# Kernel optimization log

Hardware: AMD Instinct MI355X
Metric: run time of the kernel (lower is better)

The kernel has to match this reference:

```python
import jax, jax.numpy as jnp
import numpy as np

N = 100_000   # number of local objects (rows of h_local)
E = 800_000   # number of edges (objects of class 'branch')
D = 64        # local hidden dim / out_size
DG = 16       # global hidden dim
FL = 4        # local features per edge
FG = 4        # global features
H = 128       # MLP hidden size


def setup_inputs() -> dict:
    key = jax.random.key(0)
    ks = jax.random.split(key, 20)
    inp = {}
    inp["addr_from"] = jax.random.randint(ks[0], (E,), 0, N)
    inp["addr_to"] = jax.random.randint(ks[1], (E,), 0, N)
    inp["h_local"] = jax.random.normal(ks[2], (N, D), dtype=jnp.float32)
    inp["h_global"] = jax.random.normal(ks[3], (1, DG), dtype=jnp.float32)
    inp["x_local"] = jax.random.normal(ks[4], (E, FL), dtype=jnp.float32)
    inp["x_global"] = jax.random.normal(ks[5], (1, FG), dtype=jnp.float32)
    inp["t"] = jax.random.uniform(ks[6], (1, 1), dtype=jnp.float32)
    din = 2 * D + FL + DG + FG + 1  # concat of [h_from, h_to, x_v, h_g, x_g, t]
    dims = [din, H, H, D]
    i = 7
    for pfx in ("f", "t"):  # one MLP per address field: 'from' and 'to'
        for l in range(3):
            w = (jax.random.normal(ks[i], (dims[l], dims[l + 1])) / np.sqrt(dims[l])).astype(jnp.float32)
            i += 1
            inp[f"{pfx}_W{l}"] = w
            inp[f"{pfx}_b{l}"] = jnp.zeros((dims[l + 1],), jnp.float32)
    return inp


def _mlp(x, W0, b0, W1, b1, W2, b2):
    # MLP: Dense->tanh for each hidden layer, final Dense without activation
    x = jnp.tanh(x @ W0 + b0)
    x = jnp.tanh(x @ W1 + b1)
    return x @ W2 + b2


def reference(addr_from, addr_to, h_local, h_global, x_local, x_global, t,
              f_W0, f_b0, f_W1, f_b1, f_W2, f_b2,
              t_W0, t_b0, t_W1, t_b1, t_W2, t_b2):
    ones = jnp.ones((addr_from.shape[0], 1), h_local.dtype)
    # gather_h_v_local: concat of h_local rows at each address field
    h_v = jnp.concatenate([h_local[addr_from], h_local[addr_to]], axis=1)  # [E, 2D]
    # gather_local_input: [h_v, x_v, h_g*1, x_g*1, t*1], nan_to_num
    inp = jnp.nan_to_num(
        jnp.concatenate([h_v, x_local, h_global * ones, x_global * ones, t * ones], axis=1),
        nan=0,
    )  # [E, 153]
    d_from = jnp.tanh(_mlp(inp, f_W0, f_b0, f_W1, f_b1, f_W2, f_b2))  # [E, D]
    d_to = jnp.tanh(_mlp(inp, t_W0, t_b0, t_W1, t_b1, t_W2, t_b2))    # [E, D]
    delta_sum = (0 * h_local).at[addr_from].add(d_from).at[addr_to].add(d_to)
    return jnp.tanh(delta_sum)
```

## Files before the change

kernel.cpp:

```cpp
#include <hip/hip_runtime.h>
#include <hip/hip_bf16.h>

typedef unsigned int uint;
typedef unsigned short ushort;
typedef _Float16 f16x8 __attribute__((ext_vector_type(8)));
typedef short bf16x8 __attribute__((ext_vector_type(8)));
typedef float f32x4 __attribute__((ext_vector_type(4)));
typedef uint u32x4 __attribute__((ext_vector_type(4)));

#define NE 800000
#define NN 100000
#define TE 64
#define ASTR 168
#define HSTR 136
#define SA 164
#define SH 132

#define F0_OFF 0
#define F1_OFF 20480
#define F2_OFF 36864
#define T0_OFF 45056
#define T1_OFF 65536
#define T2_OFF 81920
#define WPK_TOTAL 90112
#define WPK_BYTES (WPK_TOTAL * 2)

#define MF(a, b, c) __builtin_amdgcn_mfma_f32_16x16x32_f16(a, b, c, 0, 0, 0)

__device__ __forceinline__ float ftanh(float x) {
    float e = __builtin_amdgcn_exp2f(x * 2.885390081777927f);
    return __builtin_fmaf(-2.f, __builtin_amdgcn_rcpf(e + 1.f), 1.f);
}

__device__ __forceinline__ uint pkh(float a, float b) {
    _Float16 ha = (_Float16)a, hb = (_Float16)b;
    return (uint)__builtin_bit_cast(ushort, ha) |
           ((uint)__builtin_bit_cast(ushort, hb) << 16);
}

__device__ __forceinline__ void bfsplit(float x, ushort& hi, ushort& lo) {
    uint xb = __builtin_bit_cast(uint, x);
    hi = (ushort)(xb >> 16);
    float hif = __builtin_bit_cast(float, xb & 0xFFFF0000u);
    float res = x - hif;
    lo = (ushort)(__builtin_bit_cast(uint, res) >> 16);
}

__device__ __forceinline__ void split8(const float* v, bf16x8& fh, bf16x8& fl) {
    u32x4 H, L;
#pragma unroll
    for (int i = 0; i < 4; ++i) {
        ushort h0, l0, h1, l1;
        bfsplit(v[2*i],   h0, l0);
        bfsplit(v[2*i+1], h1, l1);
        H[i] = (uint)h0 | ((uint)h1 << 16);
        L[i] = (uint)l0 | ((uint)l1 << 16);
    }
    fh = __builtin_bit_cast(bf16x8, H);
    fl = __builtin_bit_cast(bf16x8, L);
}

__global__ __launch_bounds__(256) void pack_w(
    const float* __restrict__ fW0, const float* __restrict__ fW1, const float* __restrict__ fW2,
    const float* __restrict__ tW0, const float* __restrict__ tW1, const float* __restrict__ tW2,
    ushort* __restrict__ wpk)
{
    int idx = blockIdx.x * 256 + threadIdx.x;
    const float* src; int NP, KC, Kact, base;
    if      (idx < F1_OFF) { src = fW0; NP = 4; KC = 5; Kact = 153; base = F0_OFF; }
    else if (idx < F2_OFF) { src = fW1; NP = 4; KC = 4; Kact = 128; base = F1_OFF; }
    else if (idx < T0_OFF) { src = fW2; NP = 2; KC = 4; Kact = 128; base = F2_OFF; }
    else if (idx < T1_OFF) { src = tW0; NP = 4; KC = 5; Kact = 153; base = T0_OFF; }
    else if (idx < T2_OFF) { src = tW1; NP = 4; KC = 4; Kact = 128; base = T1_OFF; }
    else                   { src = tW2; NP = 2; KC = 4; Kact = 128; base = T2_OFF; }
    int rel  = idx - base;
    int j    = rel & 7;
    int lane = (rel >> 3) & 63;
    int sub  = rel >> 9;
    int i    = sub & 1;
    int s2   = sub >> 1;
    int kc   = s2 % KC;
    int np   = s2 / KC;
    int k = kc * 32 + ((lane >> 4) << 3) + j;
    int n = np * 32 + i * 16 + (lane & 15);
    int N = NP * 32;
    float w = (k < Kact) ? src[(size_t)k * N + n] : 0.f;
    _Float16 h = (_Float16)w;
    wpk[idx] = __builtin_bit_cast(ushort, h);
}

template<int KC>
__device__ __forceinline__ void kloop1(const ushort* __restrict__ ap, int astr,
                                       const ushort* __restrict__ gWl,
                                       f32x4 (&acc)[2][2])
{
#pragma unroll
    for (int kc = 0; kc < KC; ++kc) {
        f16x8 a0 = *(const f16x8*)(ap + kc * 32);
        f16x8 a1 = *(const f16x8*)(ap + 16 * astr + kc * 32);
        f16x8 w0 = *(const f16x8*)(gWl + kc * 1024);
        f16x8 w1 = *(const f16x8*)(gWl + kc * 1024 + 512);
        acc[0][0] = MF(a0, w0, acc[0][0]);
        acc[1][0] = MF(a1, w0, acc[1][0]);
        acc[0][1] = MF(a0, w1, acc[0][1]);
        acc[1][1] = MF(a1, w1, acc[1][1]);
    }
}

__device__ __forceinline__ void acc_init(f32x4 (&acc)[2][2],
                                         const float* __restrict__ bias,
                                         int npv, int nn)
{
#pragma unroll
    for (int ni = 0; ni < 2; ++ni) {
        float bv = bias[npv * 32 + ni * 16 + nn];
#pragma unroll
        for (int mi = 0; mi < 2; ++mi)
#pragma unroll
            for (int r = 0; r < 4; ++r) acc[mi][ni][r] = bv;
    }
}

__device__ __forceinline__ void epi_store(const f32x4 (&acc)[2][2],
                                          ushort* __restrict__ sO, int ostr,
                                          int mt, int nn, int kq, int npv)
{
#pragma unroll
    for (int mi = 0; mi < 2; ++mi)
#pragma unroll
        for (int ni = 0; ni < 2; ++ni) {
            int n = npv * 32 + ni * 16 + nn;
#pragma unroll
            for (int r = 0; r < 4; ++r) {
                int m = mt * 32 + mi * 16 + kq * 4 + r;
                _Float16 hh = (_Float16)ftanh(acc[mi][ni][r]);
                sO[m * ostr + n] = __builtin_bit_cast(ushort, hh);
            }
        }
}

__global__ __launch_bounds__(512, 6) void edge_mlp_packed(
    const int* __restrict__ af_, const int* __restrict__ at_,
    const float* __restrict__ h_local, const float* __restrict__ h_global,
    const float* __restrict__ x_local, const float* __restrict__ x_global,
    const float* __restrict__ tsc,
    const float* __restrict__ fb0, const float* __restrict__ fb1, const float* __restrict__ fb2,
    const float* __restrict__ tb0, const float* __restrict__ tb1, const float* __restrict__ tb2,
    const ushort* __restrict__ wpk, float* __restrict__ out)
{
    __shared__ ushort sAh[TE * ASTR];
    __shared__ ushort sHf[TE * HSTR];
    __shared__ int s_af[TE], s_at[TE];
    ushort* sAt = sAh;

    const int tid = threadIdx.x;
    const int e = tid >> 3, part = tid & 7;
    const int eg = blockIdx.x * TE + e;
    {
        int af = af_[eg], at = at_[eg];
        if (part == 0) { s_af[e] = af; s_at[e] = at; }
        int node = (part < 4) ? af : at;
        int k0 = ((part & 3) << 4) + ((part < 4) ? 0 : 64);
        const float4* hp = (const float4*)(h_local + (size_t)node * 64 + ((part & 3) << 4));
        float4 q0 = hp[0], q1 = hp[1], q2 = hp[2], q3 = hp[3];
        u32x4 H0, H1;
        H0[0] = pkh(q0.x, q0.y); H0[1] = pkh(q0.z, q0.w);
        H0[2] = pkh(q1.x, q1.y); H0[3] = pkh(q1.z, q1.w);
        H1[0] = pkh(q2.x, q2.y); H1[1] = pkh(q2.z, q2.w);
        H1[2] = pkh(q3.x, q3.y); H1[3] = pkh(q3.z, q3.w);
        *(u32x4*)(sAh + e * ASTR + k0)     = H0;
        *(u32x4*)(sAh + e * ASTR + k0 + 8) = H1;
        if (part < 2) {
            int k0t = 128 + part * 16;
            float w[16];
#pragma unroll
            for (int i = 0; i < 16; ++i) {
                int k = k0t + i;
                float x;
                if      (k < 132)  x = x_local[(size_t)eg * 4 + (k - 128)];
                else if (k < 148)  x = h_global[k - 132];
                else if (k < 152)  x = x_global[k - 148];
                else if (k == 152) x = tsc[0];
                else               x = 0.f;
                w[i] = x;
            }
            u32x4 H2, H3;
#pragma unroll
            for (int i = 0; i < 4; ++i) H2[i] = pkh(w[2*i], w[2*i+1]);
#pragma unroll
            for (int i = 0; i < 4; ++i) H3[i] = pkh(w[8+2*i], w[8+2*i+1]);
            *(u32x4*)(sAh + e * ASTR + k0t)     = H2;
            *(u32x4*)(sAh + e * ASTR + k0t + 8) = H3;
        }
    }
    __syncthreads();

    const int lane = tid & 63;
    const int wave = tid >> 6;
    const int mt   = wave >> 2;
    const int np   = wave & 3;
    const int nn   = lane & 15;
    const int kq   = (lane >> 4) & 3;
    const int npu  = __builtin_amdgcn_readfirstlane(np);

    const ushort* apA = sAh + (mt * 32 + nn) * ASTR + kq * 8;

    {
        f32x4 acc[2][2];
        acc_init(acc, fb0, np, nn);
        kloop1<5>(apA, ASTR, wpk + F0_OFF + npu * 5120 + lane * 8, acc);
        epi_store(acc, sHf, HSTR, mt, nn, kq, np);
    }
    {
        f32x4 acc[2][2];
        acc_init(acc, tb0, np, nn);
        kloop1<5>(apA, ASTR, wpk + T0_OFF + npu * 5120 + lane * 8, acc);
        __syncthreads();
        epi_store(acc, sAt, HSTR, mt, nn, kq, np);
    }
    __syncthreads();

    const ushort* apf = sHf + (mt * 32 + nn) * HSTR + kq * 8;
    const ushort* apt = sAt + (mt * 32 + nn) * HSTR + kq * 8;

    {
        f32x4 acc[2][2];
        acc_init(acc, fb1, np, nn);
        kloop1<4>(apf, HSTR, wpk + F1_OFF + npu * 4096 + lane * 8, acc);
        __syncthreads();
        epi_store(acc, sHf, HSTR, mt, nn, kq, np);
    }
    {
        f32x4 acc[2][2];
        acc_init(acc, tb1, np, nn);
        kloop1<4>(apt, HSTR, wpk + T1_OFF + npu * 4096 + lane * 8, acc);
        __syncthreads();
        epi_store(acc, sAt, HSTR, mt, nn, kq, np);
    }
    __syncthreads();

    {
        const int sel = __builtin_amdgcn_readfirstlane(np >> 1);
        const int np2 = __builtin_amdgcn_readfirstlane(np & 1);
        const ushort* sH  = sel ? sAt : sHf;
        const ushort* gW2 = wpk + (sel ? T2_OFF : F2_OFF) + np2 * 4096 + lane * 8;
        const float* b2   = sel ? tb2 : fb2;
        const int* nds    = sel ? s_at : s_af;

        f32x4 acc[2][2];
        acc_init(acc, b2, np2, nn);
        const ushort* ap = sH + (mt * 32 + nn) * HSTR + kq * 8;
        kloop1<4>(ap, HSTR, gW2, acc);
#pragma unroll
        for (int mi = 0; mi < 2; ++mi)
#pragma unroll
            for (int ni = 0; ni < 2; ++ni) {
                int n = np2 * 32 + ni * 16 + nn;
#pragma unroll
                for (int r = 0; r < 4; ++r) {
                    int m = mt * 32 + mi * 16 + kq * 4 + r;
                    float h = ftanh(acc[mi][ni][r]);
                    unsafeAtomicAdd(out + (size_t)nds[m] * 64 + n, h);
                }
            }
    }
}

template<int KC, int NT, int KACT, bool SCATTER>
__device__ __forceinline__ void layer(
    const float* __restrict__ sA, int astr,
    const float* __restrict__ gW, const float* __restrict__ bias,
    float* __restrict__ sO,
    float* __restrict__ out, const int* __restrict__ s_nodes, int tid)
{
    constexpr int NTW = NT / 2;
    constexpr int N = NT * 16;
    const int lane = tid & 63;
    const int wave = tid >> 6;
    const int mt   = wave >> 1;
    const int ntb  = (wave & 1) * NTW;
    const int arow = mt * 16 + (lane & 15);
    const int kg   = (lane >> 4) * 8;
    const int nn   = lane & 15;

    f32x4 aHH[NTW], aLH[NTW], aHL[NTW];
#pragma unroll
    for (int i = 0; i < NTW; ++i)
#pragma unroll
        for (int r = 0; r < 4; ++r) { aHH[i][r] = 0.f; aLH[i][r] = 0.f; aHL[i][r] = 0.f; }

#pragma unroll
    for (int kc = 0; kc < KC; ++kc) {
        const float* ap = sA + arow * astr + kc * 32 + kg;
        float av[8];
        float4 a0 = *(const float4*)ap;
        float4 a1 = *(const float4*)(ap + 4);
        av[0]=a0.x; av[1]=a0.y; av[2]=a0.z; av[3]=a0.w;
        av[4]=a1.x; av[5]=a1.y; av[6]=a1.z; av[7]=a1.w;
        bf16x8 ah, al; split8(av, ah, al);
#pragma unroll
        for (int i = 0; i < NTW; ++i) {
            int n = (ntb + i) * 16 + nn;
            float wv[8];
#pragma unroll
            for (int j = 0; j < 8; ++j) {
                int k = kc * 32 + kg + j;
                float w = 0.f;
                if (KC * 32 <= KACT || k < KACT)
                    w = gW[(size_t)k * N + n];
                wv[j] = w;
            }
            bf16x8 bh, bl; split8(wv, bh, bl);
            aHH[i] = __builtin_amdgcn_mfma_f32_16x16x32_bf16(ah, bh, aHH[i], 0, 0, 0);
            aLH[i] = __builtin_amdgcn_mfma_f32_16x16x32_bf16(al, bh, aLH[i], 0, 0, 0);
            aHL[i] = __builtin_amdgcn_mfma_f32_16x16x32_bf16(ah, bl, aHL[i], 0, 0, 0);
        }
    }

    if (!SCATTER) __syncthreads();

#pragma unroll
    for (int i = 0; i < NTW; ++i) {
        int n = (ntb + i) * 16 + nn;
        float bv = bias[n];
#pragma unroll
        for (int r = 0; r < 4; ++r) {
            int m = mt * 16 + ((lane >> 4) << 2) + r;
            float h = ftanh(aHH[i][r] + aLH[i][r] + aHL[i][r] + bv);
            if (SCATTER) {
                unsafeAtomicAdd(out + (size_t)s_nodes[m] * 64 + n, h);
            } else {
                sO[m * SH + n] = h;
            }
        }
    }
}

__global__ __launch_bounds__(512) void edge_mlp_gather(
    const int* __restrict__ af_, const int* __restrict__ at_,
    const float* __restrict__ h_local, const float* __restrict__ h_global,
    const float* __restrict__ x_local, const float* __restrict__ x_global,
    const float* __restrict__ tsc,
    const float* __restrict__ fW0, const float* __restrict__ fb0,
    const float* __restrict__ fW1, const float* __restrict__ fb1,
    const float* __restrict__ fW2, const float* __restrict__ fb2,
    const float* __restrict__ tW0, const float* __restrict__ tb0,
    const float* __restrict__ tW1, const float* __restrict__ tb1,
    const float* __restrict__ tW2, const float* __restrict__ tb2,
    float* __restrict__ out)
{
    __shared__ float sA[TE * SA];
    __shared__ float sH[TE * SH];
    __shared__ int s_af[TE], s_at[TE];

    const int tid = threadIdx.x;
    const int e = tid >> 3, part = tid & 7;
    const int eg = blockIdx.x * TE + e;
    {
        int af = af_[eg], at = at_[eg];
        if (part == 0) { s_af[e] = af; s_at[e] = at; }
        int node = (part < 4) ? af : at;
        int k0 = ((part & 3) << 4) + ((part < 4) ? 0 : 64);
        const float4* hp = (const float4*)(h_local + (size_t)node * 64 + ((part & 3) << 4));
        float4* dst = (float4*)(sA + e * SA + k0);
        dst[0] = hp[0]; dst[1] = hp[1]; dst[2] = hp[2]; dst[3] = hp[3];
        if (part < 2) {
            int k0t = 128 + part * 16;
#pragma unroll
            for (int i = 0; i < 16; ++i) {
                int k = k0t + i;
                float x;
                if      (k < 132)  x = x_local[(size_t)eg * 4 + (k - 128)];
                else if (k < 148)  x = h_global[k - 132];
                else if (k < 152)  x = x_global[k - 148];
                else if (k == 152) x = tsc[0];
                else               x = 0.f;
                sA[e * SA + k] = x;
            }
        }
    }
    __syncthreads();
    layer<5,8,153,false>(sA, SA, fW0, fb0, sH, nullptr, nullptr, tid);
    __syncthreads();
    layer<4,8,128,false>(sH, SH, fW1, fb1, sH, nullptr, nullptr, tid);
    __syncthreads();
    layer<4,4,128,true >(sH, SH, fW2, fb2, nullptr, out, s_af, tid);
    __syncthreads();
    layer<5,8,153,false>(sA, SA, tW0, tb0, sH, nullptr, nullptr, tid);
    __syncthreads();
    layer<4,8,128,false>(sH, SH, tW1, tb1, sH, nullptr, nullptr, tid);
    __syncthreads();
    layer<4,4,128,true >(sH, SH, tW2, tb2, nullptr, out, s_at, tid);
}

__global__ __launch_bounds__(256) void tanh_kernel(float* __restrict__ out, int n4) {
    int i = blockIdx.x * blockDim.x + threadIdx.x;
    int stride = gridDim.x * blockDim.x;
    float4* p = (float4*)out;
    for (; i < n4; i += stride) {
        float4 v = p[i];
        v.x = ftanh(v.x); v.y = ftanh(v.y); v.z = ftanh(v.z); v.w = ftanh(v.w);
        p[i] = v;
    }
}

extern "C" void kernel_launch(void* const* d_in, const int* in_sizes, int n_in,
                              void* d_out, int out_size, void* d_ws, size_t ws_size,
                              hipStream_t stream) {
    const int*   addr_from = (const int*)d_in[0];
    const int*   addr_to   = (const int*)d_in[1];
    const float* h_local   = (const float*)d_in[2];
    const float* h_global  = (const float*)d_in[3];
    const float* x_local   = (const float*)d_in[4];
    const float* x_global  = (const float*)d_in[5];
    const float* tsc       = (const float*)d_in[6];
    const float* fW0 = (const float*)d_in[7];
    const float* fb0 = (const float*)d_in[8];
    const float* fW1 = (const float*)d_in[9];
    const float* fb1 = (const float*)d_in[10];
    const float* fW2 = (const float*)d_in[11];
    const float* fb2 = (const float*)d_in[12];
    const float* tW0 = (const float*)d_in[13];
    const float* tb0 = (const float*)d_in[14];
    const float* tW1 = (const float*)d_in[15];
    const float* tb1 = (const float*)d_in[16];
    const float* tW2 = (const float*)d_in[17];
    const float* tb2 = (const float*)d_in[18];
    float* out = (float*)d_out;

    hipMemsetAsync(d_out, 0, (size_t)NN * 64 * sizeof(float), stream);

    if (ws_size >= (size_t)WPK_BYTES) {
        ushort* wpk = (ushort*)d_ws;
        pack_w<<<WPK_TOTAL / 256, 256, 0, stream>>>(fW0, fW1, fW2, tW0, tW1, tW2, wpk);
        edge_mlp_packed<<<NE / TE, 512, 0, stream>>>(
            addr_from, addr_to, h_local, h_global, x_local, x_global, tsc,
            fb0, fb1, fb2, tb0, tb1, tb2, wpk, out);
    } else {
        edge_mlp_gather<<<NE / TE, 512, 0, stream>>>(
            addr_from, addr_to, h_local, h_global, x_local, x_global, tsc,
            fW0, fb0, fW1, fb1, fW2, fb2, tW0, tb0, tW1, tb1, tW2, tb2, out);
    }
    tanh_kernel<<<2048, 256, 0, stream>>>(out, NN * 64 / 4);
}
```

Baseline: 394.1 us.

## Swap MFMA operand roles so each wave computes transposed tiles with vectorized epilogue

Repacks weights so each wave covers 16 edges by 64 output columns, and feeds the weight as the A operand of the MFMA so the accumulator holds 4 consecutive output columns per lane. This turns the scalar per-element LDS stores into packed 8-byte stores and lets bias loads use float4. In the final layer each lane reads one node index and issues its atomics to contiguous addresses. Each wave now loads one activation fragment and four weight fragments per k-step instead of two of each, which shifts the global/L2 weight traffic per wave.

```diff
diff --git a/kernel.cpp b/kernel.cpp
--- a/kernel.cpp
+++ b/kernel.cpp
@@ -66,77 +66,66 @@
     ushort* __restrict__ wpk)
 {
     int idx = blockIdx.x * 256 + threadIdx.x;
-    const float* src; int NP, KC, Kact, base;
-    if      (idx < F1_OFF) { src = fW0; NP = 4; KC = 5; Kact = 153; base = F0_OFF; }
-    else if (idx < F2_OFF) { src = fW1; NP = 4; KC = 4; Kact = 128; base = F1_OFF; }
-    else if (idx < T0_OFF) { src = fW2; NP = 2; KC = 4; Kact = 128; base = F2_OFF; }
-    else if (idx < T1_OFF) { src = tW0; NP = 4; KC = 5; Kact = 153; base = T0_OFF; }
-    else if (idx < T2_OFF) { src = tW1; NP = 4; KC = 4; Kact = 128; base = T1_OFF; }
-    else                   { src = tW2; NP = 2; KC = 4; Kact = 128; base = T2_OFF; }
+    const float* src; int NH, KC, Kact, base;
+    if      (idx < F1_OFF) { src = fW0; NH = 2; KC = 5; Kact = 153; base = F0_OFF; }
+    else if (idx < F2_OFF) { src = fW1; NH = 2; KC = 4; Kact = 128; base = F1_OFF; }
+    else if (idx < T0_OFF) { src = fW2; NH = 1; KC = 4; Kact = 128; base = F2_OFF; }
+    else if (idx < T1_OFF) { src = tW0; NH = 2; KC = 5; Kact = 153; base = T0_OFF; }
+    else if (idx < T2_OFF) { src = tW1; NH = 2; KC = 4; Kact = 128; base = T1_OFF; }
+    else                   { src = tW2; NH = 1; KC = 4; Kact = 128; base = T2_OFF; }
     int rel  = idx - base;
     int j    = rel & 7;
     int lane = (rel >> 3) & 63;
     int sub  = rel >> 9;
-    int i    = sub & 1;
-    int s2   = sub >> 1;
+    int i    = sub & 3;
+    int s2   = sub >> 2;
     int kc   = s2 % KC;
-    int np   = s2 / KC;
+    int nh   = s2 / KC;
     int k = kc * 32 + ((lane >> 4) << 3) + j;
-    int n = np * 32 + i * 16 + (lane & 15);
-    int N = NP * 32;
+    int n = nh * 64 + i * 16 + (lane & 15);
+    int N = NH * 64;
     float w = (k < Kact) ? src[(size_t)k * N + n] : 0.f;
     _Float16 h = (_Float16)w;
     wpk[idx] = __builtin_bit_cast(ushort, h);
 }
 
 template<int KC>
-__device__ __forceinline__ void kloop1(const ushort* __restrict__ ap, int astr,
+__device__ __forceinline__ void kloopW(const ushort* __restrict__ ap,
                                        const ushort* __restrict__ gWl,
-                                       f32x4 (&acc)[2][2])
+                                       f32x4 (&acc)[4])
 {
 #pragma unroll
     for (int kc = 0; kc < KC; ++kc) {
-        f16x8 a0 = *(const f16x8*)(ap + kc * 32);
-        f16x8 a1 = *(const f16x8*)(ap + 16 * astr + kc * 32);
-        f16x8 w0 = *(const f16x8*)(gWl + kc * 1024);
-        f16x8 w1 = *(const f16x8*)(gWl + kc * 1024 + 512);
-        acc[0][0] = MF(a0, w0, acc[0][0]);
-        acc[1][0] = MF(a1, w0, acc[1][0]);
-        acc[0][1] = MF(a0, w1, acc[0][1]);
-        acc[1][1] = MF(a1, w1, acc[1][1]);
-    }
-}
-
-__device__ __forceinline__ void acc_init(f32x4 (&acc)[2][2],
-                                         const float* __restrict__ bias,
-                                         int npv, int nn)
-{
-#pragma unroll
-    for (int ni = 0; ni < 2; ++ni) {
-        float bv = bias[npv * 32 + ni * 16 + nn];
-#pragma unroll
-        for (int mi = 0; mi < 2; ++mi)
-#pragma unroll
-            for (int r = 0; r < 4; ++r) acc[mi][ni][r] = bv;
-    }
-}
-
-__device__ __forceinline__ void epi_store(const f32x4 (&acc)[2][2],
-                                          ushort* __restrict__ sO, int ostr,
-                                          int mt, int nn, int kq, int npv)
-{
-#pragma unroll
-    for (int mi = 0; mi < 2; ++mi)
-#pragma unroll
-        for (int ni = 0; ni < 2; ++ni) {
-            int n = npv * 32 + ni * 16 + nn;
-#pragma unroll
-            for (int r = 0; r < 4; ++r) {
-                int m = mt * 32 + mi * 16 + kq * 4 + r;
-                _Float16 hh = (_Float16)ftanh(acc[mi][ni][r]);
-                sO[m * ostr + n] = __builtin_bit_cast(ushort, hh);
-            }
+        f16x8 a = *(const f16x8*)(ap + kc * 32);
+#pragma unroll
+        for (int i = 0; i < 4; ++i) {
+            f16x8 w = *(const f16x8*)(gWl + (kc * 4 + i) * 512);
+            acc[i] = MF(w, a, acc[i]);
         }
+    }
+}
+
+__device__ __forceinline__ void acc_init4(f32x4 (&acc)[4],
+                                          const float* __restrict__ bias, int nb0)
+{
+#pragma unroll
+    for (int i = 0; i < 4; ++i) {
+        float4 b = *(const float4*)(bias + nb0 + i * 16);
+        acc[i][0] = b.x; acc[i][1] = b.y; acc[i][2] = b.z; acc[i][3] = b.w;
+    }
+}
+
+__device__ __forceinline__ void epi4(const f32x4 (&acc)[4],
+                                     ushort* __restrict__ sO, int ostr,
+                                     int m, int nb0)
+{
+#pragma unroll
+    for (int i = 0; i < 4; ++i) {
+        uint2 v;
+        v.x = pkh(ftanh(acc[i][0]), ftanh(acc[i][1]));
+        v.y = pkh(ftanh(acc[i][2]), ftanh(acc[i][3]));
+        *(uint2*)(sO + m * ostr + nb0 + i * 16) = v;
+    }
 }
 
 __global__ __launch_bounds__(512, 6) void edge_mlp_packed(
@@ -155,9 +144,9 @@
 
     const int tid = threadIdx.x;
     const int e = tid >> 3, part = tid & 7;
-    const int eg = blockIdx.x * TE + e;
-    {
-        int af = af_[eg], at = at_[eg];
+    const int eg0 = blockIdx.x * TE + e;
+    {
+        int af = af_[eg0], at = at_[eg0];
         if (part == 0) { s_af[e] = af; s_at[e] = at; }
         int node = (part < 4) ? af : at;
         int k0 = ((part & 3) << 4) + ((part < 4) ? 0 : 64);
@@ -177,7 +166,7 @@
             for (int i = 0; i < 16; ++i) {
                 int k = k0t + i;
                 float x;
-                if      (k < 132)  x = x_local[(size_t)eg * 4 + (k - 128)];
+                if      (k < 132)  x = x_local[(size_t)eg0 * 4 + (k - 128)];
                 else if (k < 148)  x = h_global[k - 132];
                 else if (k < 152)  x = x_global[k - 148];
                 else if (k == 152) x = tsc[0];
@@ -197,72 +186,68 @@
 
     const int lane = tid & 63;
     const int wave = tid >> 6;
-    const int mt   = wave >> 2;
-    const int np   = wave & 3;
+    const int eg   = wave & 3;
+    const int nh   = wave >> 2;
     const int nn   = lane & 15;
     const int kq   = (lane >> 4) & 3;
-    const int npu  = __builtin_amdgcn_readfirstlane(np);
-
-    const ushort* apA = sAh + (mt * 32 + nn) * ASTR + kq * 8;
-
-    {
-        f32x4 acc[2][2];
-        acc_init(acc, fb0, np, nn);
-        kloop1<5>(apA, ASTR, wpk + F0_OFF + npu * 5120 + lane * 8, acc);
-        epi_store(acc, sHf, HSTR, mt, nn, kq, np);
-    }
-    {
-        f32x4 acc[2][2];
-        acc_init(acc, tb0, np, nn);
-        kloop1<5>(apA, ASTR, wpk + T0_OFF + npu * 5120 + lane * 8, acc);
+    const int nhu  = __builtin_amdgcn_readfirstlane(nh);
+    const int m    = eg * 16 + nn;
+    const int nb0  = nh * 64 + kq * 4;
+
+    const ushort* apA = sAh + m * ASTR + kq * 8;
+
+    {
+        f32x4 acc[4];
+        acc_init4(acc, fb0, nb0);
+        kloopW<5>(apA, wpk + F0_OFF + nhu * 10240 + lane * 8, acc);
+        epi4(acc, sHf, HSTR, m, nb0);
+    }
+    {
+        f32x4 acc[4];
+        acc_init4(acc, tb0, nb0);
+        kloopW<5>(apA, wpk + T0_OFF + nhu * 10240 + lane * 8, acc);
         __syncthreads();
-        epi_store(acc, sAt, HSTR, mt, nn, kq, np);
-    }
-    __syncthreads();
-
-    const ushort* apf = sHf + (mt * 32 + nn) * HSTR + kq * 8;
-    const ushort* apt = sAt + (mt * 32 + nn) * HSTR + kq * 8;
-
-    {
-        f32x4 acc[2][2];
-        acc_init(acc, fb1, np, nn);
-        kloop1<4>(apf, HSTR, wpk + F1_OFF + npu * 4096 + lane * 8, acc);
+        epi4(acc, sAt, HSTR, m, nb0);
+    }
+    __syncthreads();
+
+    const ushort* apf = sHf + m * HSTR + kq * 8;
+    const ushort* apt = sAt + m * HSTR + kq * 8;
+
+    {
+        f32x4 acc[4];
+        acc_init4(acc, fb1, nb0);
+        kloopW<4>(apf, wpk + F1_OFF + nhu * 8192 + lane * 8, acc);
         __syncthreads();
-        epi_store(acc, sHf, HSTR, mt, nn, kq, np);
-    }
-    {
-        f32x4 acc[2][2];
-        acc_init(acc, tb1, np, nn);
-        kloop1<4>(apt, HSTR, wpk + T1_OFF + npu * 4096 + lane * 8, acc);
+        epi4(acc, sHf, HSTR, m, nb0);
+    }
+    {
+        f32x4 acc[4];
+        acc_init4(acc, tb1, nb0);
+        kloopW<4>(apt, wpk + T1_OFF + nhu * 8192 + lane * 8, acc);
         __syncthreads();
-        epi_store(acc, sAt, HSTR, mt, nn, kq, np);
-    }
-    __syncthreads();
-
-    {
-        const int sel = __builtin_amdgcn_readfirstlane(np >> 1);
-        const int np2 = __builtin_amdgcn_readfirstlane(np & 1);
+        epi4(acc, sAt, HSTR, m, nb0);
+    }
+    __syncthreads();
+
+    {
+        const int sel = nhu;
         const ushort* sH  = sel ? sAt : sHf;
-        const ushort* gW2 = wpk + (sel ? T2_OFF : F2_OFF) + np2 * 4096 + lane * 8;
+        const ushort* gW2 = wpk + (sel ? T2_OFF : F2_OFF) + lane * 8;
         const float* b2   = sel ? tb2 : fb2;
         const int* nds    = sel ? s_at : s_af;
 
-        f32x4 acc[2][2];
-        acc_init(acc, b2, np2, nn);
-        const ushort* ap = sH + (mt * 32 + nn) * HSTR + kq * 8;
-        kloop1<4>(ap, HSTR, gW2, acc);
-#pragma unroll
-        for (int mi = 0; mi < 2; ++mi)
-#pragma unroll
-            for (int ni = 0; ni < 2; ++ni) {
-                int n = np2 * 32 + ni * 16 + nn;
-#pragma unroll
-                for (int r = 0; r < 4; ++r) {
-                    int m = mt * 32 + mi * 16 + kq * 4 + r;
-                    float h = ftanh(acc[mi][ni][r]);
-                    unsafeAtomicAdd(out + (size_t)nds[m] * 64 + n, h);
-                }
-            }
+        f32x4 acc[4];
+        acc_init4(acc, b2, kq * 4);
+        kloopW<4>(sH + m * HSTR + kq * 8, gW2, acc);
+
+        int node = nds[m];
+        float* op = out + (size_t)node * 64 + kq * 4;
+#pragma unroll
+        for (int i = 0; i < 4; ++i)
+#pragma unroll
+            for (int r = 0; r < 4; ++r)
+                unsafeAtomicAdd(op + i * 16 + r, ftanh(acc[i][r]));
     }
 }
 
```

After: 1.403 ms. +256.1%, slower.
